# Kernel tuning notes

Hardware: AMD Instinct MI355X
Metric: run time of the kernel (lower is better)

The kernel has to match this reference:

```python
import jax, jax.numpy as jnp
import numpy as np

N_NODES = 100000
N_EDGES = 3200000
N_GRAPHS = 64


def _gcn_conv(x, W, b, row, col, norm, n):
    # GCNConv: linear transform, then normalized scatter-add aggregation, then bias
    h = x @ W                                  # [N, H]
    msg = h[row] * norm[:, None]               # gather + scale, [E+N, H]
    out = jax.ops.segment_sum(msg, col, num_segments=n)
    return out + b


def setup_inputs() -> dict:
    key = jax.random.key(0)
    ks = jax.random.split(key, 8)
    x = jax.random.normal(ks[0], (N_NODES, 128), dtype=jnp.float32)
    edge_index = jax.random.randint(ks[1], (2, N_EDGES), 0, N_NODES, dtype=jnp.int64)
    batch = jnp.sort(jax.random.randint(ks[2], (N_NODES,), 0, N_GRAPHS, dtype=jnp.int64))
    W1 = jax.random.normal(ks[3], (128, 256), dtype=jnp.float32) * (1.0 / np.sqrt(128))
    b1 = jnp.zeros((256,), dtype=jnp.float32)
    W2 = jax.random.normal(ks[4], (256, 256), dtype=jnp.float32) * (1.0 / np.sqrt(256))
    b2 = jnp.zeros((256,), dtype=jnp.float32)
    Wl = jax.random.normal(ks[5], (256, 2), dtype=jnp.float32) * (1.0 / np.sqrt(256))
    bl = jnp.zeros((2,), dtype=jnp.float32)
    return {"x": x, "edge_index": edge_index, "batch": batch,
            "W1": W1, "b1": b1, "W2": W2, "b2": b2, "Wl": Wl, "bl": bl}


def reference(x, edge_index, batch, W1, b1, W2, b2, Wl, bl):
    n = x.shape[0]
    # add self-loops (PyG GCNConv default)
    loop = jnp.arange(n, dtype=edge_index.dtype)
    row = jnp.concatenate([edge_index[0], loop])   # source
    col = jnp.concatenate([edge_index[1], loop])   # target
    # symmetric normalization: deg computed on targets (with self-loops)
    deg = jax.ops.segment_sum(jnp.ones_like(col, dtype=x.dtype), col, num_segments=n)
    dinv = jnp.where(deg > 0, jax.lax.rsqrt(deg), 0.0)
    norm = dinv[row] * dinv[col]

    h = jax.nn.relu(_gcn_conv(x, W1, b1, row, col, norm, n))
    # dropout p=0.1 is identity at inference (training=False)
    h = jax.nn.relu(_gcn_conv(h, W2, b2, row, col, norm, n))

    # global mean pool over graphs
    sums = jax.ops.segment_sum(h, batch, num_segments=N_GRAPHS)
    cnts = jax.ops.segment_sum(jnp.ones((n,), dtype=h.dtype), batch, num_segments=N_GRAPHS)
    pooled = sums / jnp.maximum(cnts, 1.0)[:, None]

    return pooled @ Wl + bl
```

## Files before the change

### kernel.cpp

```cpp
#include <hip/hip_runtime.h>
#include <hip/hip_bf16.h>
#include <cstddef>

#define NODES  100000
#define EDGES  3200000
#define ETOT   3300000
#define NGRAPH 64
#define HDIM   256
#define BSHIFT 9
#define NBUCK  196
#define BCAP   19456

typedef __hip_bfloat16 bf16;
typedef short bf16x8 __attribute__((ext_vector_type(8)));
typedef float f32x4 __attribute__((ext_vector_type(4)));
typedef float f32x2 __attribute__((ext_vector_type(2)));
typedef unsigned u32x2 __attribute__((ext_vector_type(2)));
typedef unsigned u32x4 __attribute__((ext_vector_type(4)));

__global__ void xcast_kernel(const float* __restrict__ x, unsigned char* __restrict__ x8) {
    int i = blockIdx.x * 256 + threadIdx.x;
    if ((size_t)i * 4 >= (size_t)NODES * 128) return;
    float4 v = *(const float4*)(x + (size_t)i * 4);
    int w = __builtin_amdgcn_cvt_pk_fp8_f32(v.x, v.y, 0, false);
    w     = __builtin_amdgcn_cvt_pk_fp8_f32(v.z, v.w, w, true);
    *(unsigned*)(x8 + (size_t)i * 4) = (unsigned)w;
}

__global__ void wcast_kernel(const float* __restrict__ W1, const float* __restrict__ W2,
                             bf16* __restrict__ W1t, bf16* __restrict__ W2t) {
    int i = blockIdx.x * 256 + threadIdx.x;
    if (i < 128 * 256) {
        int n = i / 128, k = i - n * 128;
        W1t[i] = __float2bfloat16(W1[(size_t)k * 256 + n]);
    } else if (i < 128 * 256 + 256 * 256) {
        int q = i - 128 * 256;
        int n = q / 256, k = q - n * 256;
        W2t[q] = __float2bfloat16(W2[(size_t)k * 256 + n]);
    }
}

__global__ __launch_bounds__(1024) void fillp1_kernel(const int* __restrict__ row,
                                                      const int* __restrict__ col,
                                                      int* __restrict__ gcnt,
                                                      uint2* __restrict__ recs) {
    __shared__ int hist[4][NBUCK];
    __shared__ int coff[4][NBUCK];
    __shared__ int base[NBUCK];
    int t  = threadIdx.x;
    int cp = t & 3;
    for (int i = t; i < 4 * NBUCK; i += 1024) ((int*)hist)[i] = 0;
    __syncthreads();
    int e0 = blockIdx.x * 16384;
    int r[16], c[16], rk[16];
    #pragma unroll
    for (int i = 0; i < 16; i++) {
        int e = e0 + i * 1024 + t;
        r[i] = -1;
        if (e < ETOT) {
            if (e < EDGES) { r[i] = row[e]; c[i] = col[e]; }
            else           { r[i] = e - EDGES; c[i] = r[i]; }
            rk[i] = atomicAdd(&hist[cp][c[i] >> BSHIFT], 1);
        }
    }
    __syncthreads();
    if (t < NBUCK) {
        int h0 = hist[0][t], h1 = hist[1][t], h2 = hist[2][t], h3 = hist[3][t];
        coff[0][t] = 0; coff[1][t] = h0; coff[2][t] = h0 + h1; coff[3][t] = h0 + h1 + h2;
        int tot = h0 + h1 + h2 + h3;
        base[t] = (tot > 0) ? atomicAdd(&gcnt[t], tot) : 0;
    }
    __syncthreads();
    #pragma unroll
    for (int i = 0; i < 16; i++) {
        if (r[i] >= 0) {
            int b = c[i] >> BSHIFT;
            recs[(size_t)b * BCAP + base[b] + coff[cp][b] + rk[i]] =
                make_uint2((unsigned)r[i], (unsigned)c[i]);
        }
    }
}

__global__ void bscan_kernel(const int* __restrict__ gcnt, int* __restrict__ bbase) {
    __shared__ int part[256];
    int t = threadIdx.x;
    int v0 = (t < NBUCK) ? gcnt[t] : 0;
    part[t] = v0;
    __syncthreads();
    for (int off = 1; off < 256; off <<= 1) {
        int v = (t >= off) ? part[t - off] : 0;
        __syncthreads();
        part[t] += v;
        __syncthreads();
    }
    if (t < NBUCK) bbase[t] = part[t] - v0;
}

__global__ __launch_bounds__(256) void build_kernel(const uint2* __restrict__ recs,
                                                    const int* __restrict__ gcnt,
                                                    const int* __restrict__ bbase,
                                                    int* __restrict__ rowptr,
                                                    float* __restrict__ dinv,
                                                    int* __restrict__ csr) {
    __shared__ int hist[512];
    __shared__ int cur[512];
    __shared__ int part[256];
    const int b = blockIdx.x, t = threadIdx.x;
    const int n0 = b << BSHIFT;
    const int cnt = gcnt[b];
    const int base = bbase[b];
    hist[t] = 0; hist[t + 256] = 0;
    __syncthreads();
    const uint2* rb = recs + (size_t)b * BCAP;
    for (int i = t; i < cnt; i += 256) atomicAdd(&hist[(int)rb[i].y - n0], 1);
    __syncthreads();
    int h0 = hist[2 * t], h1 = hist[2 * t + 1];
    part[t] = h0 + h1;
    __syncthreads();
    for (int off = 1; off < 256; off <<= 1) {
        int v = (t >= off) ? part[t - off] : 0;
        __syncthreads();
        part[t] += v;
        __syncthreads();
    }
    int ex = (t == 0) ? 0 : part[t - 1];
    cur[2 * t]     = ex;
    cur[2 * t + 1] = ex + h0;
    int v0 = n0 + 2 * t, v1 = v0 + 1;
    if (v0 < NODES) { rowptr[v0] = base + ex;      dinv[v0] = rsqrtf((float)h0); }
    if (v1 < NODES) { rowptr[v1] = base + ex + h0; dinv[v1] = rsqrtf((float)h1); }
    if (b == 0 && t == 0) rowptr[NODES] = ETOT;
    __syncthreads();
    for (int i = t; i < cnt; i += 256) {
        uint2 r = rb[i];
        int pos = atomicAdd(&cur[(int)r.y - n0], 1);
        csr[base + pos] = (int)r.x;
    }
}

__global__ void agg1_kernel(const unsigned char* __restrict__ x8, const int* __restrict__ rowptr,
                            const int* __restrict__ csr, const float* __restrict__ dinv,
                            bf16* __restrict__ out) {
    int w    = (blockIdx.x * blockDim.x + threadIdx.x) >> 6;
    int lane = threadIdx.x & 63;
    int half = lane >> 5, li = lane & 31;
    int node = w * 2 + half;
    if (node >= NODES) return;
    int beg = rowptr[node], end = rowptr[node + 1];
    float a0 = 0.f, a1 = 0.f, a2 = 0.f, a3 = 0.f;
    int j = beg;
#define ACC4(q, wv) do {                                                   \
        f32x2 d0 = __builtin_amdgcn_cvt_pk_f32_fp8((int)(q), false);       \
        f32x2 d1 = __builtin_amdgcn_cvt_pk_f32_fp8((int)(q), true);        \
        a0 += (wv) * d0.x; a1 += (wv) * d0.y;                              \
        a2 += (wv) * d1.x; a3 += (wv) * d1.y;                              \
    } while (0)
    for (; j + 3 < end; j += 4) {
        int s0 = csr[j], s1 = csr[j + 1], s2 = csr[j + 2], s3 = csr[j + 3];
        float w0 = dinv[s0], w1 = dinv[s1], w2 = dinv[s2], w3 = dinv[s3];
        unsigned q0 = *(const unsigned*)(x8 + (size_t)s0 * 128 + li * 4);
        unsigned q1 = *(const unsigned*)(x8 + (size_t)s1 * 128 + li * 4);
        unsigned q2 = *(const unsigned*)(x8 + (size_t)s2 * 128 + li * 4);
        unsigned q3 = *(const unsigned*)(x8 + (size_t)s3 * 128 + li * 4);
        ACC4(q0, w0); ACC4(q1, w1); ACC4(q2, w2); ACC4(q3, w3);
    }
    for (; j < end; j++) {
        int s0 = csr[j];
        float w0 = dinv[s0];
        unsigned q0 = *(const unsigned*)(x8 + (size_t)s0 * 128 + li * 4);
        ACC4(q0, w0);
    }
#undef ACC4
    float d = dinv[node];
    union { __hip_bfloat162 h[2]; u32x2 u; } pk;
    pk.h[0] = __float22bfloat162_rn(make_float2(a0 * d, a1 * d));
    pk.h[1] = __float22bfloat162_rn(make_float2(a2 * d, a3 * d));
    *(u32x2*)(out + (size_t)node * 128 + li * 4) = pk.u;
}

__global__ void agg2_kernel(const unsigned char* __restrict__ h8, const int* __restrict__ rowptr,
                            const int* __restrict__ csr, const float* __restrict__ dinv,
                            bf16* __restrict__ out) {
    int w    = (blockIdx.x * blockDim.x + threadIdx.x) >> 6;
    int lane = threadIdx.x & 63;
    int half = lane >> 5, li = lane & 31;
    int node = w * 2 + half;
    if (node >= NODES) return;
    int beg = rowptr[node], end = rowptr[node + 1];
    float a[8] = {};
    int j = beg;
#define ACC8(q, wv) do {                                                   \
        f32x2 d0 = __builtin_amdgcn_cvt_pk_f32_fp8((int)(q).x, false);     \
        f32x2 d1 = __builtin_amdgcn_cvt_pk_f32_fp8((int)(q).x, true);      \
        f32x2 d2 = __builtin_amdgcn_cvt_pk_f32_fp8((int)(q).y, false);     \
        f32x2 d3 = __builtin_amdgcn_cvt_pk_f32_fp8((int)(q).y, true);      \
        a[0] += (wv) * d0.x; a[1] += (wv) * d0.y;                          \
        a[2] += (wv) * d1.x; a[3] += (wv) * d1.y;                          \
        a[4] += (wv) * d2.x; a[5] += (wv) * d2.y;                          \
        a[6] += (wv) * d3.x; a[7] += (wv) * d3.y;                          \
    } while (0)
    for (; j + 3 < end; j += 4) {
        int s0 = csr[j], s1 = csr[j + 1], s2 = csr[j + 2], s3 = csr[j + 3];
        float w0 = dinv[s0], w1 = dinv[s1], w2 = dinv[s2], w3 = dinv[s3];
        u32x2 q0 = *(const u32x2*)(h8 + (size_t)s0 * 256 + li * 8);
        u32x2 q1 = *(const u32x2*)(h8 + (size_t)s1 * 256 + li * 8);
        u32x2 q2 = *(const u32x2*)(h8 + (size_t)s2 * 256 + li * 8);
        u32x2 q3 = *(const u32x2*)(h8 + (size_t)s3 * 256 + li * 8);
        ACC8(q0, w0); ACC8(q1, w1); ACC8(q2, w2); ACC8(q3, w3);
    }
    for (; j < end; j++) {
        int s0 = csr[j];
        float w0 = dinv[s0];
        u32x2 q0 = *(const u32x2*)(h8 + (size_t)s0 * 256 + li * 8);
        ACC8(q0, w0);
    }
#undef ACC8
    float d = dinv[node];
    union { __hip_bfloat162 h[4]; u32x4 u; } pk;
    pk.h[0] = __float22bfloat162_rn(make_float2(a[0] * d, a[1] * d));
    pk.h[1] = __float22bfloat162_rn(make_float2(a[2] * d, a[3] * d));
    pk.h[2] = __float22bfloat162_rn(make_float2(a[4] * d, a[5] * d));
    pk.h[3] = __float22bfloat162_rn(make_float2(a[6] * d, a[7] * d));
    *(u32x4*)(out + (size_t)node * 256 + li * 8) = pk.u;
}

template <int K>
__global__ __launch_bounds__(256) void mgemm_kernel(const bf16* __restrict__ A,
                                                    const bf16* __restrict__ Bt,
                                                    const float* __restrict__ bias,
                                                    unsigned char* __restrict__ C8) {
    __shared__ short As[128][40];
    __shared__ short Bs[128][40];
    const int t    = threadIdx.x;
    const int bm   = (int)(blockIdx.x >> 1) * 128;
    const int bn   = (int)(blockIdx.x & 1) * 128;
    const int lane = t & 63;
    const int wave = t >> 6;
    const int wm   = (wave >> 1) * 64, wn = (wave & 1) * 64;
    const int m16  = lane & 15, kq = lane >> 4;
    f32x4 acc[4][4] = {};

    for (int k0 = 0; k0 < K; k0 += 32) {
        #pragma unroll
        for (int h = 0; h < 2; h++) {
            int q = t * 2 + h;
            int rr = q >> 2, seg = q & 3;
            uint4 va = {0u, 0u, 0u, 0u};
            int grow = bm + rr;
            if (grow < NODES) va = *(const uint4*)(A + (size_t)grow * K + k0 + seg * 8);
            *(uint4*)&As[rr][seg * 8] = va;
            uint4 vb = *(const uint4*)(Bt + (size_t)(bn + rr) * K + k0 + seg * 8);
            *(uint4*)&Bs[rr][seg * 8] = vb;
        }
        __syncthreads();
        bf16x8 af[4], bf_[4];
        #pragma unroll
        for (int i = 0; i < 4; i++) {
            af[i]  = *(const bf16x8*)&As[wm + i * 16 + m16][kq * 8];
            bf_[i] = *(const bf16x8*)&Bs[wn + i * 16 + m16][kq * 8];
        }
        #pragma unroll
        for (int mt = 0; mt < 4; mt++)
            #pragma unroll
            for (int nt = 0; nt < 4; nt++)
                acc[mt][nt] = __builtin_amdgcn_mfma_f32_16x16x32_bf16(af[mt], bf_[nt],
                                                                     acc[mt][nt], 0, 0, 0);
        __syncthreads();
    }

    #pragma unroll
    for (int mt = 0; mt < 4; mt++) {
        #pragma unroll
        for (int r = 0; r < 4; r++) {
            int row = bm + wm + mt * 16 + kq * 4 + r;
            if (row >= NODES) continue;
            #pragma unroll
            for (int nt = 0; nt < 4; nt++) {
                int colb = bn + wn + nt * 16 + m16;
                float v = fmaxf(acc[mt][nt][r] + bias[colb], 0.f);
                int pkd = __builtin_amdgcn_cvt_pk_fp8_f32(v, v, 0, false);
                C8[(size_t)row * 256 + colb] = (unsigned char)(pkd & 0xff);
            }
        }
    }
}

__global__ void pool_kernel(const unsigned char* __restrict__ h2, const int* __restrict__ batch,
                            float* __restrict__ sums) {
    int lane = threadIdx.x & 63;
    int sub  = threadIdx.x >> 6;
    int r0   = blockIdx.x * 1024 + sub * 256;
    if (r0 >= NODES) return;
    int r1 = r0 + 256; if (r1 > NODES) r1 = NODES;
    float a0 = 0.f, a1 = 0.f, a2 = 0.f, a3 = 0.f;
    int g = batch[r0];
    int cb = lane * 4;
    for (int r = r0; r < r1; r++) {
        int gg = batch[r];
        if (gg != g) {
            atomicAdd(&sums[g * 256 + cb + 0], a0);
            atomicAdd(&sums[g * 256 + cb + 1], a1);
            atomicAdd(&sums[g * 256 + cb + 2], a2);
            atomicAdd(&sums[g * 256 + cb + 3], a3);
            a0 = a1 = a2 = a3 = 0.f; g = gg;
        }
        unsigned q = *(const unsigned*)(h2 + (size_t)r * 256 + cb);
        f32x2 d0 = __builtin_amdgcn_cvt_pk_f32_fp8((int)q, false);
        f32x2 d1 = __builtin_amdgcn_cvt_pk_f32_fp8((int)q, true);
        a0 += d0.x; a1 += d0.y; a2 += d1.x; a3 += d1.y;
    }
    atomicAdd(&sums[g * 256 + cb + 0], a0);
    atomicAdd(&sums[g * 256 + cb + 1], a1);
    atomicAdd(&sums[g * 256 + cb + 2], a2);
    atomicAdd(&sums[g * 256 + cb + 3], a3);
}

__global__ void final_kernel(const float* __restrict__ sums, const int* __restrict__ batch,
                             const float* __restrict__ Wl, const float* __restrict__ bl,
                             float* __restrict__ out) {
    int g = blockIdx.x;
    int l = threadIdx.x;
    int lo = 0, hi = NODES;
    while (lo < hi) { int m = (lo + hi) >> 1; if (batch[m] < g) lo = m + 1; else hi = m; }
    int lb = lo;
    lo = lb; hi = NODES;
    while (lo < hi) { int m = (lo + hi) >> 1; if (batch[m] <= g) lo = m + 1; else hi = m; }
    int cnt = lo - lb;
    float inv = 1.f / fmaxf((float)cnt, 1.f);
    float a0 = 0.f, a1 = 0.f;
    for (int k = l; k < 256; k += 64) {
        float p = sums[g * 256 + k] * inv;
        a0 += p * Wl[k * 2 + 0];
        a1 += p * Wl[k * 2 + 1];
    }
    for (int off = 32; off > 0; off >>= 1) {
        a0 += __shfl_down(a0, off, 64);
        a1 += __shfl_down(a1, off, 64);
    }
    if (l == 0) {
        out[g * 2 + 0] = a0 + bl[0];
        out[g * 2 + 1] = a1 + bl[1];
    }
}

extern "C" void kernel_launch(void* const* d_in, const int* in_sizes, int n_in,
                              void* d_out, int out_size, void* d_ws, size_t ws_size,
                              hipStream_t stream) {
    const float* x    = (const float*)d_in[0];
    const int*   ei   = (const int*)d_in[1];
    const int*   bat  = (const int*)d_in[2];
    const float* W1   = (const float*)d_in[3];
    const float* b1   = (const float*)d_in[4];
    const float* W2   = (const float*)d_in[5];
    const float* b2   = (const float*)d_in[6];
    const float* Wl   = (const float*)d_in[7];
    const float* bl   = (const float*)d_in[8];
    float*       out  = (float*)d_out;
    const int* erow = ei;
    const int* ecol = ei + EDGES;

    char* p = (char*)d_ws;
    auto take = [&](size_t bytes) {
        char* r = p;
        p += (bytes + 255) & ~(size_t)255;
        return r;
    };
    float* dinv   = (float*)take((size_t)NODES * 4);
    int*   rowptr = (int*)  take((size_t)(NODES + 1) * 4);
    int*   gcnt   = (int*)  take((size_t)NBUCK * 4);
    int*   bbase  = (int*)  take((size_t)NBUCK * 4);
    int*   csr    = (int*)  take((size_t)ETOT * 4);
    float* sums   = (float*)take((size_t)NGRAPH * HDIM * 4);
    bf16*  W1t    = (bf16*) take((size_t)128 * 256 * 2);
    bf16*  W2t    = (bf16*) take((size_t)256 * 256 * 2);
    char*  reg1   = (char*) take((size_t)NODES * HDIM * 1);
    char*  reg2   = (char*) take((size_t)NODES * HDIM * 2);
    char*  reg3   = (char*) take((size_t)NBUCK * BCAP * 8);
    unsigned char* x8      = (unsigned char*)reg1;
    unsigned char* h1f8    = (unsigned char*)reg1;
    bf16*          aggbuf1 = (bf16*)reg2;
    bf16*          aggbuf2 = (bf16*)reg2;
    uint2*         recs    = (uint2*)reg3;
    unsigned char* h2f8    = (unsigned char*)reg3;

    hipMemsetAsync(sums, 0, (size_t)NGRAPH * HDIM * 4, stream);
    hipMemsetAsync(gcnt, 0, (size_t)NBUCK * 4, stream);
    xcast_kernel<<<(NODES * 128 / 4 + 255) / 256, 256, 0, stream>>>(x, x8);
    wcast_kernel<<<(128 * 256 + 256 * 256 + 255) / 256, 256, 0, stream>>>(W1, W2, W1t, W2t);

    fillp1_kernel<<<(ETOT + 16383) / 16384, 1024, 0, stream>>>(erow, ecol, gcnt, recs);
    bscan_kernel <<<1, 256, 0, stream>>>(gcnt, bbase);
    build_kernel <<<NBUCK, 256, 0, stream>>>(recs, gcnt, bbase, rowptr, dinv, csr);

    const int AGG_BLOCKS = (NODES / 2 * 64) / 256;
    agg1_kernel<<<AGG_BLOCKS, 256, 0, stream>>>(x8, rowptr, csr, dinv, aggbuf1);

    const int MB = (NODES + 127) / 128;
    mgemm_kernel<128><<<MB * 2, 256, 0, stream>>>(aggbuf1, W1t, b1, h1f8);

    agg2_kernel<<<AGG_BLOCKS, 256, 0, stream>>>(h1f8, rowptr, csr, dinv, aggbuf2);

    mgemm_kernel<256><<<MB * 2, 256, 0, stream>>>(aggbuf2, W2t, b2, h2f8);

    pool_kernel<<<(NODES + 1023) / 1024, 256, 0, stream>>>(h2f8, bat, sums);

    final_kernel<<<NGRAPH, 64, 0, stream>>>(sums, bat, Wl, bl, out);
}
```

Baseline: 560.8 us.

## Prescale source features by dinv and pack bucket records into 32 bits

Source-side normalization is folded into the producers: xcast scales x by dinv before the fp8 cast, and the first GEMM epilogue scales its output by dinv[row]. This removes the per-edge dinv gather from both aggregation kernels. Edge bucket records also shrink from 8-byte (row,col) pairs to one 32-bit word holding the source and the local target offset, which halves bucket traffic. The cost is that xcast must now wait for the CSR build, and fp8 quantization now sees pre-scaled values, which slightly changes rounding.

```diff
diff --git a/kernel.cpp b/kernel.cpp
--- a/kernel.cpp
+++ b/kernel.cpp
@@ -18,12 +18,14 @@
 typedef unsigned u32x2 __attribute__((ext_vector_type(2)));
 typedef unsigned u32x4 __attribute__((ext_vector_type(4)));
 
-__global__ void xcast_kernel(const float* __restrict__ x, unsigned char* __restrict__ x8) {
+__global__ void xcast_kernel(const float* __restrict__ x, const float* __restrict__ dinv,
+                             unsigned char* __restrict__ x8) {
     int i = blockIdx.x * 256 + threadIdx.x;
     if ((size_t)i * 4 >= (size_t)NODES * 128) return;
+    float d = dinv[i >> 5];
     float4 v = *(const float4*)(x + (size_t)i * 4);
-    int w = __builtin_amdgcn_cvt_pk_fp8_f32(v.x, v.y, 0, false);
-    w     = __builtin_amdgcn_cvt_pk_fp8_f32(v.z, v.w, w, true);
+    int w = __builtin_amdgcn_cvt_pk_fp8_f32(v.x * d, v.y * d, 0, false);
+    w     = __builtin_amdgcn_cvt_pk_fp8_f32(v.z * d, v.w * d, w, true);
     *(unsigned*)(x8 + (size_t)i * 4) = (unsigned)w;
 }
 
@@ -43,7 +45,7 @@
 __global__ __launch_bounds__(1024) void fillp1_kernel(const int* __restrict__ row,
                                                       const int* __restrict__ col,
                                                       int* __restrict__ gcnt,
-                                                      uint2* __restrict__ recs) {
+                                                      unsigned* __restrict__ recs) {
     __shared__ int hist[4][NBUCK];
     __shared__ int coff[4][NBUCK];
     __shared__ int base[NBUCK];
@@ -76,7 +78,7 @@
         if (r[i] >= 0) {
             int b = c[i] >> BSHIFT;
             recs[(size_t)b * BCAP + base[b] + coff[cp][b] + rk[i]] =
-                make_uint2((unsigned)r[i], (unsigned)c[i]);
+                ((unsigned)r[i] << BSHIFT) | (unsigned)(c[i] & 511);
         }
     }
 }
@@ -96,7 +98,7 @@
     if (t < NBUCK) bbase[t] = part[t] - v0;
 }
 
-__global__ __launch_bounds__(256) void build_kernel(const uint2* __restrict__ recs,
+__global__ __launch_bounds__(256) void build_kernel(const unsigned* __restrict__ recs,
                                                     const int* __restrict__ gcnt,
                                                     const int* __restrict__ bbase,
                                                     int* __restrict__ rowptr,
@@ -106,13 +108,13 @@
     __shared__ int cur[512];
     __shared__ int part[256];
     const int b = blockIdx.x, t = threadIdx.x;
-    const int n0 = b << BSHIFT;
     const int cnt = gcnt[b];
     const int base = bbase[b];
+    const int n0 = b << BSHIFT;
     hist[t] = 0; hist[t + 256] = 0;
     __syncthreads();
-    const uint2* rb = recs + (size_t)b * BCAP;
-    for (int i = t; i < cnt; i += 256) atomicAdd(&hist[(int)rb[i].y - n0], 1);
+    const unsigned* rb = recs + (size_t)b * BCAP;
+    for (int i = t; i < cnt; i += 256) atomicAdd(&hist[rb[i] & 511u], 1);
     __syncthreads();
     int h0 = hist[2 * t], h1 = hist[2 * t + 1];
     part[t] = h0 + h1;
@@ -132,9 +134,9 @@
     if (b == 0 && t == 0) rowptr[NODES] = ETOT;
     __syncthreads();
     for (int i = t; i < cnt; i += 256) {
-        uint2 r = rb[i];
-        int pos = atomicAdd(&cur[(int)r.y - n0], 1);
-        csr[base + pos] = (int)r.x;
+        unsigned r = rb[i];
+        int pos = atomicAdd(&cur[r & 511u], 1);
+        csr[base + pos] = (int)(r >> BSHIFT);
     }
 }
 
@@ -149,26 +151,22 @@
     int beg = rowptr[node], end = rowptr[node + 1];
     float a0 = 0.f, a1 = 0.f, a2 = 0.f, a3 = 0.f;
     int j = beg;
-#define ACC4(q, wv) do {                                                   \
+#define ACC4(q) do {                                                       \
         f32x2 d0 = __builtin_amdgcn_cvt_pk_f32_fp8((int)(q), false);       \
         f32x2 d1 = __builtin_amdgcn_cvt_pk_f32_fp8((int)(q), true);        \
-        a0 += (wv) * d0.x; a1 += (wv) * d0.y;                              \
-        a2 += (wv) * d1.x; a3 += (wv) * d1.y;                              \
+        a0 += d0.x; a1 += d0.y; a2 += d1.x; a3 += d1.y;                    \
     } while (0)
     for (; j + 3 < end; j += 4) {
         int s0 = csr[j], s1 = csr[j + 1], s2 = csr[j + 2], s3 = csr[j + 3];
-        float w0 = dinv[s0], w1 = dinv[s1], w2 = dinv[s2], w3 = dinv[s3];
         unsigned q0 = *(const unsigned*)(x8 + (size_t)s0 * 128 + li * 4);
         unsigned q1 = *(const unsigned*)(x8 + (size_t)s1 * 128 + li * 4);
         unsigned q2 = *(const unsigned*)(x8 + (size_t)s2 * 128 + li * 4);
         unsigned q3 = *(const unsigned*)(x8 + (size_t)s3 * 128 + li * 4);
-        ACC4(q0, w0); ACC4(q1, w1); ACC4(q2, w2); ACC4(q3, w3);
+        ACC4(q0); ACC4(q1); ACC4(q2); ACC4(q3);
     }
     for (; j < end; j++) {
-        int s0 = csr[j];
-        float w0 = dinv[s0];
-        unsigned q0 = *(const unsigned*)(x8 + (size_t)s0 * 128 + li * 4);
-        ACC4(q0, w0);
+        unsigned q0 = *(const unsigned*)(x8 + (size_t)csr[j] * 128 + li * 4);
+        ACC4(q0);
     }
 #undef ACC4
     float d = dinv[node];
@@ -189,30 +187,25 @@
     int beg = rowptr[node], end = rowptr[node + 1];
     float a[8] = {};
     int j = beg;
-#define ACC8(q, wv) do {                                                   \
+#define ACC8(q) do {                                                       \
         f32x2 d0 = __builtin_amdgcn_cvt_pk_f32_fp8((int)(q).x, false);     \
         f32x2 d1 = __builtin_amdgcn_cvt_pk_f32_fp8((int)(q).x, true);      \
         f32x2 d2 = __builtin_amdgcn_cvt_pk_f32_fp8((int)(q).y, false);     \
         f32x2 d3 = __builtin_amdgcn_cvt_pk_f32_fp8((int)(q).y, true);      \
-        a[0] += (wv) * d0.x; a[1] += (wv) * d0.y;                          \
-        a[2] += (wv) * d1.x; a[3] += (wv) * d1.y;                          \
-        a[4] += (wv) * d2.x; a[5] += (wv) * d2.y;                          \
-        a[6] += (wv) * d3.x; a[7] += (wv) * d3.y;                          \
+        a[0] += d0.x; a[1] += d0.y; a[2] += d1.x; a[3] += d1.y;            \
+        a[4] += d2.x; a[5] += d2.y; a[6] += d3.x; a[7] += d3.y;            \
     } while (0)
     for (; j + 3 < end; j += 4) {
         int s0 = csr[j], s1 = csr[j + 1], s2 = csr[j + 2], s3 = csr[j + 3];
-        float w0 = dinv[s0], w1 = dinv[s1], w2 = dinv[s2], w3 = dinv[s3];
         u32x2 q0 = *(const u32x2*)(h8 + (size_t)s0 * 256 + li * 8);
         u32x2 q1 = *(const u32x2*)(h8 + (size_t)s1 * 256 + li * 8);
         u32x2 q2 = *(const u32x2*)(h8 + (size_t)s2 * 256 + li * 8);
         u32x2 q3 = *(const u32x2*)(h8 + (size_t)s3 * 256 + li * 8);
-        ACC8(q0, w0); ACC8(q1, w1); ACC8(q2, w2); ACC8(q3, w3);
+        ACC8(q0); ACC8(q1); ACC8(q2); ACC8(q3);
     }
     for (; j < end; j++) {
-        int s0 = csr[j];
-        float w0 = dinv[s0];
-        u32x2 q0 = *(const u32x2*)(h8 + (size_t)s0 * 256 + li * 8);
-        ACC8(q0, w0);
+        u32x2 q0 = *(const u32x2*)(h8 + (size_t)csr[j] * 256 + li * 8);
+        ACC8(q0);
     }
 #undef ACC8
     float d = dinv[node];
@@ -224,10 +217,11 @@
     *(u32x4*)(out + (size_t)node * 256 + li * 8) = pk.u;
 }
 
-template <int K>
+template <int K, bool PRESCALE>
 __global__ __launch_bounds__(256) void mgemm_kernel(const bf16* __restrict__ A,
                                                     const bf16* __restrict__ Bt,
                                                     const float* __restrict__ bias,
+                                                    const float* __restrict__ dinv,
                                                     unsigned char* __restrict__ C8) {
     __shared__ short As[128][40];
     __shared__ short Bs[128][40];
@@ -274,10 +268,11 @@
         for (int r = 0; r < 4; r++) {
             int row = bm + wm + mt * 16 + kq * 4 + r;
             if (row >= NODES) continue;
+            float sc = PRESCALE ? dinv[row] : 1.f;
             #pragma unroll
             for (int nt = 0; nt < 4; nt++) {
                 int colb = bn + wn + nt * 16 + m16;
-                float v = fmaxf(acc[mt][nt][r] + bias[colb], 0.f);
+                float v = fmaxf(acc[mt][nt][r] + bias[colb], 0.f) * sc;
                 int pkd = __builtin_amdgcn_cvt_pk_fp8_f32(v, v, 0, false);
                 C8[(size_t)row * 256 + colb] = (unsigned char)(pkd & 0xff);
             }
@@ -375,32 +370,33 @@
     bf16*  W2t    = (bf16*) take((size_t)256 * 256 * 2);
     char*  reg1   = (char*) take((size_t)NODES * HDIM * 1);
     char*  reg2   = (char*) take((size_t)NODES * HDIM * 2);
-    char*  reg3   = (char*) take((size_t)NBUCK * BCAP * 8);
+    char*  reg3   = (char*) take((size_t)NODES * HDIM * 1);
     unsigned char* x8      = (unsigned char*)reg1;
     unsigned char* h1f8    = (unsigned char*)reg1;
     bf16*          aggbuf1 = (bf16*)reg2;
     bf16*          aggbuf2 = (bf16*)reg2;
-    uint2*         recs    = (uint2*)reg3;
+    unsigned*      recs    = (unsigned*)reg3;
     unsigned char* h2f8    = (unsigned char*)reg3;
 
     hipMemsetAsync(sums, 0, (size_t)NGRAPH * HDIM * 4, stream);
     hipMemsetAsync(gcnt, 0, (size_t)NBUCK * 4, stream);
-    xcast_kernel<<<(NODES * 128 / 4 + 255) / 256, 256, 0, stream>>>(x, x8);
     wcast_kernel<<<(128 * 256 + 256 * 256 + 255) / 256, 256, 0, stream>>>(W1, W2, W1t, W2t);
 
     fillp1_kernel<<<(ETOT + 16383) / 16384, 1024, 0, stream>>>(erow, ecol, gcnt, recs);
     bscan_kernel <<<1, 256, 0, stream>>>(gcnt, bbase);
     build_kernel <<<NBUCK, 256, 0, stream>>>(recs, gcnt, bbase, rowptr, dinv, csr);
 
+    xcast_kernel<<<(NODES * 128 / 4 + 255) / 256, 256, 0, stream>>>(x, dinv, x8);
+
     const int AGG_BLOCKS = (NODES / 2 * 64) / 256;
     agg1_kernel<<<AGG_BLOCKS, 256, 0, stream>>>(x8, rowptr, csr, dinv, aggbuf1);
 
     const int MB = (NODES + 127) / 128;
-    mgemm_kernel<128><<<MB * 2, 256, 0, stream>>>(aggbuf1, W1t, b1, h1f8);
+    mgemm_kernel<128, true ><<<MB * 2, 256, 0, stream>>>(aggbuf1, W1t, b1, dinv, h1f8);
 
     agg2_kernel<<<AGG_BLOCKS, 256, 0, stream>>>(h1f8, rowptr, csr, dinv, aggbuf2);
 
-    mgemm_kernel<256><<<MB * 2, 256, 0, stream>>>(aggbuf2, W2t, b2, h2f8);
+    mgemm_kernel<256, false><<<MB * 2, 256, 0, stream>>>(aggbuf2, W2t, b2, nullptr, h2f8);
 
     pool_kernel<<<(NODES + 1023) / 1024, 256, 0, stream>>>(h2f8, bat, sums);
 
```

Result: no change. 555.8 us (-0.9%).
